# Kernel optimization log

Measured on AMD Instinct MI355X. Metric: run time of the kernel, lower is better.

The kernel has to match this reference:

```python
import jax, jax.numpy as jnp
import numpy as np
import math

THETA = 10000.0
NUM_HEADS = 16


def apply_rope(x, pos, theta):
    # x: [B, H, S, Dh], pos: [S]
    d_k = x.shape[-1]
    inv_freq = theta ** (-jnp.arange(0, d_k, 2, dtype=x.dtype) / d_k)  # [Dh/2]
    angles = pos.astype(x.dtype)[:, None] * inv_freq  # [S, Dh/2]
    cos = jnp.cos(angles)
    sin = jnp.sin(angles)
    x_even = x[..., ::2]
    x_odd = x[..., 1::2]
    out_even = x_even * cos - x_odd * sin
    out_odd = x_even * sin + x_odd * cos
    # interleave back: stack on trailing axis then flatten
    return jnp.stack((out_even, out_odd), axis=-1).reshape(x.shape)


def setup_inputs() -> dict:
    key = jax.random.key(0)
    ks = jax.random.split(key, 5)
    B, S, D = 2, 2048, 1024
    scale = 1.0 / math.sqrt(D)
    return {
        "in_features": jax.random.normal(ks[0], (B, S, D), dtype=jnp.float32),
        "token_positions": jnp.arange(S, dtype=jnp.int64 if jax.config.jax_enable_x64 else jnp.int32),
        "Wq": jax.random.normal(ks[1], (D, D), dtype=jnp.float32) * scale,
        "Wk": jax.random.normal(ks[2], (D, D), dtype=jnp.float32) * scale,
        "Wv": jax.random.normal(ks[3], (D, D), dtype=jnp.float32) * scale,
        "Wo": jax.random.normal(ks[4], (D, D), dtype=jnp.float32) * scale,
    }


def reference(in_features, token_positions, Wq, Wk, Wv, Wo):
    B, S, D = in_features.shape
    H = NUM_HEADS
    Dh = D // H

    def split_heads(x):  # [B,S,D] -> [B,H,S,Dh]
        return x.reshape(B, S, H, Dh).transpose(0, 2, 1, 3)

    # nn.Linear convention: y = x @ W.T
    q = split_heads(in_features @ Wq.T)
    k = split_heads(in_features @ Wk.T)
    v = split_heads(in_features @ Wv.T)

    q = apply_rope(q, token_positions, THETA)
    k = apply_rope(k, token_positions, THETA)

    scores = jnp.einsum('bhqd,bhkd->bhqk', q, k) / jnp.sqrt(jnp.asarray(Dh, q.dtype))
    causal = jnp.tril(jnp.ones((S, S), dtype=bool))
    scores = jnp.where(causal, scores, jnp.asarray(-jnp.inf, scores.dtype))
    weights = jax.nn.softmax(scores, axis=-1)
    out = jnp.einsum('bhqk,bhkd->bhqd', weights, v)  # [B,H,S,Dh]
    out = out.transpose(0, 2, 1, 3).reshape(B, S, D)
    return out @ Wo.T
```

## Files before the change

### kernel.cpp

```cpp
#include <hip/hip_runtime.h>
#include <hip/hip_bf16.h>


typedef __bf16 bf16x8 __attribute__((ext_vector_type(8)));
typedef float floatx4 __attribute__((ext_vector_type(4)));
typedef float floatx16 __attribute__((ext_vector_type(16)));
typedef int intx2 __attribute__((ext_vector_type(2)));

#define MFMA16(A, B, C) __builtin_amdgcn_mfma_f32_16x16x32_bf16((A), (B), (C), 0, 0, 0)
#define MFMA32(A, B, C) __builtin_amdgcn_mfma_f32_32x32x16_bf16((A), (B), (C), 0, 0, 0)

#define S_LEN 2048
#define D_MODEL 1024
#define NHEAD 16
#define DHEAD 64
#define NTOK 4096
#define NEG_SENTINEL (-1.0e30f)
#define QSCALE_LOG2E 0.18033688011112042f

__device__ __forceinline__ short b16(float f) {
  __bf16 h = (__bf16)f;
  union { __bf16 b; short s; } u; u.b = h;
  return u.s;
}
__device__ __forceinline__ unsigned pk2(float x, float y) {
  union { __bf16 b[2]; unsigned u; } t;
  t.b[0] = (__bf16)x; t.b[1] = (__bf16)y;
  return t.u;
}
__device__ __forceinline__ bf16x8 ld_frag(const short* p) {
  return *(const bf16x8*)p;
}
__device__ __forceinline__ void gl2lds16(const short* g, short* l) {
  __builtin_amdgcn_global_load_lds(
      (const __attribute__((address_space(1))) unsigned int*)g,
      (__attribute__((address_space(3))) unsigned int*)l, 16, 0, 0);
}
__device__ __forceinline__ float max3f(float a, float b, float c) {
  return fmaxf(fmaxf(a, b), c);
}

__global__ __launch_bounds__(256) void prep_kernel(
    const float* __restrict__ x, const float* __restrict__ wq,
    const float* __restrict__ wk, const float* __restrict__ wv,
    short* __restrict__ xb, short* __restrict__ wqb,
    short* __restrict__ wkb, short* __restrict__ wvb,
    float2* __restrict__ tab) {
  const int y = blockIdx.y;
  if (y == 4) {
    int i = blockIdx.x * 256 + threadIdx.x;
    int s = i >> 5, p = i & 31;
    float inv_freq = __expf(-0.28782313662425575f * (float)p);
    float ang = (float)s * inv_freq;
    float sn, c;
    sincosf(ang, &sn, &c);
    tab[i] = make_float2(c, sn);
    return;
  }
  const float* src = (y == 0) ? x : (y == 1) ? wq : (y == 2) ? wk : wv;
  short* dst = (y == 0) ? xb : (y == 1) ? wqb : (y == 2) ? wkb : wvb;
  const int n4 = ((y == 0) ? NTOK * D_MODEL : D_MODEL * D_MODEL) >> 2;
  for (int i = blockIdx.x * 256 + threadIdx.x; i < n4; i += gridDim.x * 256) {
    float4 v = ((const float4*)src)[i];
    short4 o;
    o.x = b16(v.x); o.y = b16(v.y); o.z = b16(v.z); o.w = b16(v.w);
    ((short4*)dst)[i] = o;
  }
}

__global__ __launch_bounds__(256) void qkv_rope_kernel(
    const short* __restrict__ xb,
    const short* __restrict__ Wqb, const short* __restrict__ Wkb,
    const short* __restrict__ Wvb,
    const float2* __restrict__ ropetab,
    short* __restrict__ qws, short* __restrict__ kws, short* __restrict__ vtws) {
  __shared__ __align__(16) short SM[4 * 64 * 72];
  short* As = SM;
  short* Bs = SM + 128 * 64;

  const int tid = threadIdx.x;
  const int lane = tid & 63;
  const int wv = tid >> 6;
  const int col = lane & 15, quad = lane >> 4;
  const int half = lane >> 5, l31 = lane & 31;
  const int wr = wv >> 1, wc = wv & 1;
  const int gemm = blockIdx.y;
  const int bm = blockIdx.x >> 3;
  const int bn = blockIdx.x & 7;
  const short* W = (gemm == 0) ? Wqb : (gemm == 1) ? Wkb : Wvb;

  const int srow8 = lane >> 3;
  const int scolsw = ((lane & 7) ^ srow8) * 8;
  const short* gAa[4]; short* lAa[4];
  const short* gBa[4]; short* lBa[4];
#pragma unroll
  for (int g = 0; g < 2; ++g)
#pragma unroll
    for (int j = 0; j < 2; ++j) {
      const int idx = g * 2 + j;
      const int r0 = g * 64 + wv * 16 + j * 8;
      gAa[idx] = xb + (size_t)(bm * 128 + r0 + srow8) * D_MODEL + scolsw;
      lAa[idx] = As + r0 * 64;
      gBa[idx] = W + (size_t)(bn * 128 + r0 + srow8) * D_MODEL + scolsw;
      lBa[idx] = Bs + r0 * 64;
    }

  floatx4 acc[4][4];
#pragma unroll
  for (int i = 0; i < 4; ++i)
#pragma unroll
    for (int j = 0; j < 4; ++j) acc[i][j] = (floatx4){0.f, 0.f, 0.f, 0.f};

  const int arow = wr * 64;
  const int brow = wc * 64;

  for (int k0 = 0; k0 < D_MODEL; k0 += 64) {
    __syncthreads();
#pragma unroll
    for (int i = 0; i < 4; ++i) gl2lds16(gAa[i] + k0, lAa[i]);
#pragma unroll
    for (int i = 0; i < 4; ++i) gl2lds16(gBa[i] + k0, lBa[i]);
    __syncthreads();
#pragma unroll
    for (int kk = 0; kk < 2; ++kk) {
      bf16x8 a[4], b[4];
      const int usel = (kk * 4 + quad) ^ (col & 7);
#pragma unroll
      for (int mt = 0; mt < 4; ++mt)
        a[mt] = ld_frag(&As[(arow + mt * 16 + col) * 64 + usel * 8]);
#pragma unroll
      for (int nt = 0; nt < 4; ++nt)
        b[nt] = ld_frag(&Bs[(brow + nt * 16 + col) * 64 + usel * 8]);
#pragma unroll
      for (int mt = 0; mt < 4; ++mt)
#pragma unroll
        for (int nt = 0; nt < 4; ++nt)
          acc[mt][nt] = MFMA16(a[mt], b[nt], acc[mt][nt]);
    }
  }
  __syncthreads();

  const int tm = bm * 2 + wr;
  const int tn = bn * 2 + wc;
  short* Ep = &SM[wv * 64 * 72];
  const int mbase = tm * 64;
  const int bb = mbase >> 11;
  const int s0 = mbase & (S_LEN - 1);

  if (gemm == 2) {
#pragma unroll
    for (int mt = 0; mt < 4; ++mt)
#pragma unroll
      for (int nt = 0; nt < 4; ++nt) {
        int nl = nt * 16 + col;
#pragma unroll
        for (int r = 0; r < 4; ++r)
          Ep[nl * 72 + mt * 16 + quad * 4 + r] = b16(acc[mt][nt][r]);
      }
    short* vb2 = vtws + (size_t)(bb * NHEAD + tn) * S_LEN * DHEAD;
    const int vtile = s0 >> 6;
#pragma unroll
    for (int dt = 0; dt < 2; ++dt) {
      const int4* src = (const int4*)&Ep[(dt * 32 + l31) * 72];
      int4* dst = (int4*)(vb2 + (size_t)(vtile * 8 + dt) * 512);
#pragma unroll
      for (int kc = 0; kc < 4; ++kc)
        dst[kc * 2 * 64 + lane] = src[kc * 2 + half];
    }
  } else {
    short* outp = (gemm == 0) ? qws : kws;
    const float qscale = (gemm == 0) ? QSCALE_LOG2E : 1.0f;
#pragma unroll
    for (int nt = 0; nt < 4; ++nt) {
      int nl = nt * 16 + col;
      const float2* tp = ropetab + (nl >> 1);
#pragma unroll
      for (int mt = 0; mt < 4; ++mt)
#pragma unroll
        for (int r = 0; r < 4; ++r) {
          int ml = mt * 16 + quad * 4 + r;
          float2 cs = tp[(size_t)(s0 + ml) * 32];
          float val = acc[mt][nt][r];
          float partner = __shfl_xor(val, 1);
          float o = ((nl & 1) == 0) ? (val * cs.x - partner * cs.y)
                                    : (partner * cs.y + val * cs.x);
          Ep[ml * 72 + nl] = b16(o * qscale);
        }
    }
    short* ob2 = outp + (size_t)(bb * NHEAD + tn) * S_LEN * DHEAD;
    const int kgrp0 = s0 >> 5;
#pragma unroll
    for (int g2 = 0; g2 < 2; ++g2) {
      const int4* src = (const int4*)&Ep[(g2 * 32 + l31) * 72];
      int4* dst = (int4*)(ob2 + (size_t)((kgrp0 + g2) * 4) * 512);
#pragma unroll
      for (int kc = 0; kc < 4; ++kc)
        dst[kc * 64 + lane] = src[kc * 2 + half];
    }
  }
}

__global__ __launch_bounds__(256) void attn_kernel(
    const short* __restrict__ qws, const short* __restrict__ kws,
    const short* __restrict__ vtws, short* __restrict__ att) {
  const int tid = threadIdx.x;
  const int wv = tid >> 6;
  const int lane = tid & 63;
  const int half = lane >> 5, l31 = lane & 31;
  const int bh = blockIdx.x & 31;
  const int b = bh >> 4, h = bh & 15;
  const int qt = 63 - (blockIdx.x >> 5);
  const int q0 = qt * 32;

  __shared__ float ml[2][4][32];
  __shared__ float Obuf[4][64][33];

  const short* qbase = qws + (size_t)(b * NHEAD + h) * S_LEN * DHEAD;
  const short* kbase = kws + (size_t)(b * NHEAD + h) * S_LEN * DHEAD;
  const short* vbase = vtws + (size_t)(b * NHEAD + h) * S_LEN * DHEAD;

  bf16x8 qf[4];
#pragma unroll
  for (int kc = 0; kc < 4; ++kc)
    qf[kc] = ld_frag(qbase + (size_t)(qt * 4 + kc) * 512 + lane * 8);

  float m_i = NEG_SENTINEL, l_i = 0.f;
  floatx16 ot[2] = {};

  const int nit = (q0 + 32 + 63) >> 6;

  bf16x8 kfA[2][4];
  auto loadK = [&](int tkt) {
#pragma unroll
    for (int s = 0; s < 2; ++s) {
      if (tkt + s * 32 <= q0 + 31) {
        const short* kr = kbase + (size_t)(((tkt >> 5) + s) * 4) * 512 + lane * 8;
#pragma unroll
        for (int kc = 0; kc < 4; ++kc) kfA[s][kc] = ld_frag(kr + kc * 512);
      }
    }
  };

  int it = wv;
  if (it < nit) loadK(it * 64);

  for (; it < nit; it += 4) {
    const int kt = it * 64;
    bf16x8 vf[4][2];
    {
      const short* vr = vbase + (size_t)(kt >> 6) * 8 * 512 + lane * 8;
#pragma unroll
      for (int kc = 0; kc < 4; ++kc)
#pragma unroll
        for (int dt = 0; dt < 2; ++dt)
          vf[kc][dt] = ld_frag(vr + (size_t)(kc * 2 + dt) * 512);
    }
    floatx16 sc[2];
#pragma unroll
    for (int s = 0; s < 2; ++s) {
      if (kt + s * 32 <= q0 + 31) {
        floatx16 a = {};
#pragma unroll
        for (int kc = 0; kc < 4; ++kc) a = MFMA32(kfA[s][kc], qf[kc], a);
        sc[s] = a;
      } else {
#pragma unroll
        for (int rg = 0; rg < 16; ++rg) sc[s][rg] = NEG_SENTINEL;
      }
    }
    if (it + 4 < nit) loadK((it + 4) * 64);

    if (kt + 63 > q0) {
      const int lim = q0 + l31 - kt;
#pragma unroll
      for (int s = 0; s < 2; ++s)
#pragma unroll
        for (int rg = 0; rg < 16; ++rg) {
          int rel = s * 32 + (rg & 3) + 8 * (rg >> 2) + 4 * half;
          if (rel > lim) sc[s][rg] = NEG_SENTINEL;
        }
    }
    float u[11];
#pragma unroll
    for (int j = 0; j < 10; ++j)
      u[j] = max3f(((const float*)&sc[0])[3 * j],
                   ((const float*)&sc[0])[3 * j + 1],
                   ((const float*)&sc[0])[3 * j + 2]);
    u[10] = fmaxf(((const float*)&sc[0])[30], ((const float*)&sc[0])[31]);
    float w0 = max3f(u[0], u[1], u[2]);
    float w1 = max3f(u[3], u[4], u[5]);
    float w2 = max3f(u[6], u[7], u[8]);
    float w3 = fmaxf(u[9], u[10]);
    float rm = fmaxf(fmaxf(w0, w1), fmaxf(w2, w3));

    if (!__all(rm <= m_i + 8.0f)) {
      float rmf = fmaxf(rm, __shfl_xor(rm, 32));
      float mnew = fmaxf(m_i, rmf);
      float alpha = exp2f(m_i - mnew);
      m_i = mnew;
      l_i *= alpha;
#pragma unroll
      for (int dt = 0; dt < 2; ++dt)
#pragma unroll
        for (int rg = 0; rg < 16; ++rg) ot[dt][rg] *= alpha;
    }

    unsigned pw[8][2];
    float rsp[8];
#pragma unroll
    for (int s = 0; s < 2; ++s)
#pragma unroll
      for (int g = 0; g < 4; ++g) {
        float p0 = exp2f(sc[s][4 * g + 0] - m_i);
        float p1 = exp2f(sc[s][4 * g + 1] - m_i);
        float p2 = exp2f(sc[s][4 * g + 2] - m_i);
        float p3 = exp2f(sc[s][4 * g + 3] - m_i);
        rsp[s * 4 + g] = (p0 + p1) + (p2 + p3);
        pw[s * 4 + g][0] = pk2(p0, p1);
        pw[s * 4 + g][1] = pk2(p2, p3);
      }
    float rs = ((rsp[0] + rsp[1]) + (rsp[2] + rsp[3])) +
               ((rsp[4] + rsp[5]) + (rsp[6] + rsp[7]));
    rs += __shfl_xor(rs, 32);
    l_i += rs;

#pragma unroll
    for (int kc = 0; kc < 4; ++kc) {
      intx2 s01 = __builtin_amdgcn_permlane32_swap(
          (int)pw[2 * kc][0], (int)pw[2 * kc + 1][0], false, false);
      intx2 s23 = __builtin_amdgcn_permlane32_swap(
          (int)pw[2 * kc][1], (int)pw[2 * kc + 1][1], false, false);
      union { unsigned u[4]; bf16x8 f; } fr;
      fr.u[0] = (unsigned)s01[0]; fr.u[1] = (unsigned)s23[0];
      fr.u[2] = (unsigned)s01[1]; fr.u[3] = (unsigned)s23[1];
#pragma unroll
      for (int dt = 0; dt < 2; ++dt)
        ot[dt] = MFMA32(vf[kc][dt], fr.f, ot[dt]);
    }
  }

  ml[0][wv][l31] = m_i;
  ml[1][wv][l31] = l_i;
  __syncthreads();
  float m0 = ml[0][0][l31], m1 = ml[0][1][l31];
  float m2 = ml[0][2][l31], m3 = ml[0][3][l31];
  float mtot = fmaxf(fmaxf(m0, m1), fmaxf(m2, m3));
  float sw = exp2f(m_i - mtot);

#pragma unroll
  for (int dt = 0; dt < 2; ++dt)
#pragma unroll
    for (int rg = 0; rg < 16; ++rg) {
      int d = dt * 32 + (rg & 3) + 8 * (rg >> 2) + 4 * half;
      Obuf[wv][d][l31] = ot[dt][rg] * sw;
    }
  __syncthreads();

  const int q = tid >> 3;
  const int d0 = (tid & 7) * 8;
  float mm0 = ml[0][0][q], mm1 = ml[0][1][q], mm2 = ml[0][2][q], mm3 = ml[0][3][q];
  float mt2 = fmaxf(fmaxf(mm0, mm1), fmaxf(mm2, mm3));
  float lt = ml[1][0][q] * exp2f(mm0 - mt2) + ml[1][1][q] * exp2f(mm1 - mt2) +
             ml[1][2][q] * exp2f(mm2 - mt2) + ml[1][3][q] * exp2f(mm3 - mt2);
  float inv = 1.0f / lt;
  union { bf16x8 hh; int4 i4; } cv;
#pragma unroll
  for (int i = 0; i < 8; ++i) {
    float v = ((Obuf[0][d0 + i][q] + Obuf[1][d0 + i][q]) +
               (Obuf[2][d0 + i][q] + Obuf[3][d0 + i][q]));
    cv.hh[i] = (__bf16)(v * inv);
  }
  int4* dst = (int4*)(att + (size_t)(b * S_LEN + q0 + q) * D_MODEL + h * DHEAD + d0);
  *dst = cv.i4;
}

__global__ __launch_bounds__(256) void out_gemm_kernel(
    const short* __restrict__ att, const float* __restrict__ Wo,
    float* __restrict__ out) {
  __shared__ __align__(16) short As[128 * 64];
  __shared__ __align__(16) short Bs[64 * 64];

  const int tid = threadIdx.x;
  const int lane = tid & 63;
  const int wv = tid >> 6;
  const int col = lane & 15, quad = lane >> 4;
  const int wr = wv >> 1, wc = wv & 1;
  const int bm = blockIdx.x >> 4;
  const int bn = blockIdx.x & 15;

  const int srow8 = lane >> 3;
  const int scolsw = ((lane & 7) ^ srow8) * 8;
  const short* gAa[4]; short* lAa[4];
#pragma unroll
  for (int g = 0; g < 2; ++g)
#pragma unroll
    for (int j = 0; j < 2; ++j) {
      const int idx = g * 2 + j;
      const int r0 = g * 64 + wv * 16 + j * 8;
      gAa[idx] = att + (size_t)(bm * 128 + r0 + srow8) * D_MODEL + scolsw;
      lAa[idx] = As + r0 * 64;
    }

  const int browB = tid >> 2;
  const int bc0 = (tid & 3) * 16;
  const float* gBf = Wo + (size_t)(bn * 64 + browB) * D_MODEL + bc0;
  short* lBw0 = Bs + browB * 64 + (((tid & 3) * 2) ^ (browB & 7)) * 8;
  short* lBw1 = Bs + browB * 64 + (((tid & 3) * 2 + 1) ^ (browB & 7)) * 8;

  floatx4 acc[4][2];
#pragma unroll
  for (int i = 0; i < 4; ++i)
#pragma unroll
    for (int j = 0; j < 2; ++j) acc[i][j] = (floatx4){0.f, 0.f, 0.f, 0.f};

  const int arow = wr * 64;
  const int brow = wc * 32;

  for (int k0 = 0; k0 < D_MODEL; k0 += 64) {
    float4 w0 = *(const float4*)(gBf + k0);
    float4 w1 = *(const float4*)(gBf + k0 + 4);
    float4 w2 = *(const float4*)(gBf + k0 + 8);
    float4 w3 = *(const float4*)(gBf + k0 + 12);
    __syncthreads();
#pragma unroll
    for (int i = 0; i < 4; ++i) gl2lds16(gAa[i] + k0, lAa[i]);
    union { unsigned u[4]; int4 i4; } b0, b1;
    b0.u[0] = pk2(w0.x, w0.y); b0.u[1] = pk2(w0.z, w0.w);
    b0.u[2] = pk2(w1.x, w1.y); b0.u[3] = pk2(w1.z, w1.w);
    b1.u[0] = pk2(w2.x, w2.y); b1.u[1] = pk2(w2.z, w2.w);
    b1.u[2] = pk2(w3.x, w3.y); b1.u[3] = pk2(w3.z, w3.w);
    *(int4*)lBw0 = b0.i4;
    *(int4*)lBw1 = b1.i4;
    __syncthreads();
#pragma unroll
    for (int kk = 0; kk < 2; ++kk) {
      bf16x8 a[4], b[2];
      const int usel = (kk * 4 + quad) ^ (col & 7);
#pragma unroll
      for (int mt = 0; mt < 4; ++mt)
        a[mt] = ld_frag(&As[(arow + mt * 16 + col) * 64 + usel * 8]);
#pragma unroll
      for (int nt = 0; nt < 2; ++nt)
        b[nt] = ld_frag(&Bs[(brow + nt * 16 + col) * 64 + usel * 8]);
#pragma unroll
      for (int mt = 0; mt < 4; ++mt)
#pragma unroll
        for (int nt = 0; nt < 2; ++nt)
          acc[mt][nt] = MFMA16(a[mt], b[nt], acc[mt][nt]);
    }
  }

#pragma unroll
  for (int mt = 0; mt < 4; ++mt)
#pragma unroll
    for (int nt = 0; nt < 2; ++nt) {
      int n = bn * 64 + wc * 32 + nt * 16 + col;
#pragma unroll
      for (int r = 0; r < 4; ++r) {
        int m = bm * 128 + wr * 64 + mt * 16 + quad * 4 + r;
        out[(size_t)m * D_MODEL + n] = acc[mt][nt][r];
      }
    }
}

extern "C" void kernel_launch(void* const* d_in, const int* in_sizes, int n_in,
                              void* d_out, int out_size, void* d_ws, size_t ws_size,
                              hipStream_t stream) {
  const float* x  = (const float*)d_in[0];
  const float* Wq = (const float*)d_in[2];
  const float* Wk = (const float*)d_in[3];
  const float* Wv = (const float*)d_in[4];
  const float* Wo = (const float*)d_in[5];
  float* out = (float*)d_out;

  const size_t TENS = (size_t)NTOK * D_MODEL;
  const size_t WELEM = (size_t)D_MODEL * D_MODEL;

  short* qws  = (short*)d_out;
  short* xb   = (short*)d_out + TENS;
  short* kws  = (short*)d_ws;
  short* vtws = kws + TENS;
  short* attws = vtws + TENS;
  short* wqb = attws;
  short* wkb = wqb + WELEM;
  short* wvb = wkb + WELEM;
  float2* ropetab = (float2*)(wvb + WELEM);

  prep_kernel<<<dim3(256, 5), 256, 0, stream>>>(x, Wq, Wk, Wv, xb, wqb, wkb, wvb, ropetab);
  qkv_rope_kernel<<<dim3(256, 3), 256, 0, stream>>>(xb, wqb, wkb, wvb, ropetab, qws, kws, vtws);
  attn_kernel<<<dim3(2048), 256, 0, stream>>>(qws, kws, vtws, attws);
  out_gemm_kernel<<<dim3(512), 256, 0, stream>>>(attws, Wo, out);
}
```

Baseline: 191.3 us.

## Split attention inner loop into two 32-key phases and halve LDS output buffer

The 64-key iteration of the attention kernel is restructured into two 32-key sub-phases, each computing scores, online softmax and PV MFMAs separately. V fragments are loaded per phase, which lowers live register pressure and interleaves the next K prefetch with each half. The cross-wave output reduction now uses a two-slot LDS buffer with an extra barrier and accumulate step, halving shared memory. The cost is more softmax rescale checks, extra shuffles per tile and one more synchronisation.

```diff
diff --git a/kernel.cpp b/kernel.cpp
--- a/kernel.cpp
+++ b/kernel.cpp
@@ -213,7 +213,7 @@
   const int q0 = qt * 32;
 
   __shared__ float ml[2][4][32];
-  __shared__ float Obuf[4][64][33];
+  __shared__ float Obuf[2][64][33];
 
   const short* qbase = qws + (size_t)(b * NHEAD + h) * S_LEN * DHEAD;
   const short* kbase = kws + (size_t)(b * NHEAD + h) * S_LEN * DHEAD;
@@ -230,69 +230,28 @@
   const int nit = (q0 + 32 + 63) >> 6;
 
   bf16x8 kfA[2][4];
-  auto loadK = [&](int tkt) {
-#pragma unroll
-    for (int s = 0; s < 2; ++s) {
-      if (tkt + s * 32 <= q0 + 31) {
-        const short* kr = kbase + (size_t)(((tkt >> 5) + s) * 4) * 512 + lane * 8;
-#pragma unroll
-        for (int kc = 0; kc < 4; ++kc) kfA[s][kc] = ld_frag(kr + kc * 512);
-      }
+  auto loadKs = [&](int s, int tkt) {
+    if (tkt + s * 32 <= q0 + 31) {
+      const short* kr = kbase + (size_t)(((tkt >> 5) + s) * 4) * 512 + lane * 8;
+#pragma unroll
+      for (int kc = 0; kc < 4; ++kc) kfA[s][kc] = ld_frag(kr + kc * 512);
     }
   };
 
-  int it = wv;
-  if (it < nit) loadK(it * 64);
-
-  for (; it < nit; it += 4) {
-    const int kt = it * 64;
-    bf16x8 vf[4][2];
-    {
-      const short* vr = vbase + (size_t)(kt >> 6) * 8 * 512 + lane * 8;
-#pragma unroll
-      for (int kc = 0; kc < 4; ++kc)
-#pragma unroll
-        for (int dt = 0; dt < 2; ++dt)
-          vf[kc][dt] = ld_frag(vr + (size_t)(kc * 2 + dt) * 512);
-    }
-    floatx16 sc[2];
-#pragma unroll
-    for (int s = 0; s < 2; ++s) {
-      if (kt + s * 32 <= q0 + 31) {
-        floatx16 a = {};
-#pragma unroll
-        for (int kc = 0; kc < 4; ++kc) a = MFMA32(kfA[s][kc], qf[kc], a);
-        sc[s] = a;
-      } else {
-#pragma unroll
-        for (int rg = 0; rg < 16; ++rg) sc[s][rg] = NEG_SENTINEL;
-      }
-    }
-    if (it + 4 < nit) loadK((it + 4) * 64);
-
-    if (kt + 63 > q0) {
-      const int lim = q0 + l31 - kt;
-#pragma unroll
-      for (int s = 0; s < 2; ++s)
-#pragma unroll
-        for (int rg = 0; rg < 16; ++rg) {
-          int rel = s * 32 + (rg & 3) + 8 * (rg >> 2) + 4 * half;
-          if (rel > lim) sc[s][rg] = NEG_SENTINEL;
-        }
-    }
-    float u[11];
-#pragma unroll
-    for (int j = 0; j < 10; ++j)
-      u[j] = max3f(((const float*)&sc[0])[3 * j],
-                   ((const float*)&sc[0])[3 * j + 1],
-                   ((const float*)&sc[0])[3 * j + 2]);
-    u[10] = fmaxf(((const float*)&sc[0])[30], ((const float*)&sc[0])[31]);
-    float w0 = max3f(u[0], u[1], u[2]);
-    float w1 = max3f(u[3], u[4], u[5]);
-    float w2 = max3f(u[6], u[7], u[8]);
-    float w3 = fmaxf(u[9], u[10]);
-    float rm = fmaxf(fmaxf(w0, w1), fmaxf(w2, w3));
-
+  auto phase = [&](floatx16 sc, int kbase_rel, const short* vr) {
+    bf16x8 vfp[2][2];
+#pragma unroll
+    for (int kcg = 0; kcg < 2; ++kcg)
+#pragma unroll
+      for (int dt = 0; dt < 2; ++dt)
+        vfp[kcg][dt] = ld_frag(vr + (size_t)(kcg * 2 + dt) * 512);
+    const float* sf = (const float*)&sc;
+    float u0 = max3f(sf[0], sf[1], sf[2]);
+    float u1 = max3f(sf[3], sf[4], sf[5]);
+    float u2 = max3f(sf[6], sf[7], sf[8]);
+    float u3 = max3f(sf[9], sf[10], sf[11]);
+    float u4 = max3f(sf[12], sf[13], sf[14]);
+    float rm = fmaxf(max3f(u0, u1, u2), max3f(u3, u4, sf[15]));
     if (!__all(rm <= m_i + 8.0f)) {
       float rmf = fmaxf(rm, __shfl_xor(rm, 32));
       float mnew = fmaxf(m_i, rmf);
@@ -304,38 +263,75 @@
 #pragma unroll
         for (int rg = 0; rg < 16; ++rg) ot[dt][rg] *= alpha;
     }
-
-    unsigned pw[8][2];
-    float rsp[8];
-#pragma unroll
-    for (int s = 0; s < 2; ++s)
-#pragma unroll
-      for (int g = 0; g < 4; ++g) {
-        float p0 = exp2f(sc[s][4 * g + 0] - m_i);
-        float p1 = exp2f(sc[s][4 * g + 1] - m_i);
-        float p2 = exp2f(sc[s][4 * g + 2] - m_i);
-        float p3 = exp2f(sc[s][4 * g + 3] - m_i);
-        rsp[s * 4 + g] = (p0 + p1) + (p2 + p3);
-        pw[s * 4 + g][0] = pk2(p0, p1);
-        pw[s * 4 + g][1] = pk2(p2, p3);
-      }
-    float rs = ((rsp[0] + rsp[1]) + (rsp[2] + rsp[3])) +
-               ((rsp[4] + rsp[5]) + (rsp[6] + rsp[7]));
+    unsigned pw[4][2];
+    float rsp[4];
+#pragma unroll
+    for (int g = 0; g < 4; ++g) {
+      float p0 = exp2f(sc[4 * g + 0] - m_i);
+      float p1 = exp2f(sc[4 * g + 1] - m_i);
+      float p2 = exp2f(sc[4 * g + 2] - m_i);
+      float p3 = exp2f(sc[4 * g + 3] - m_i);
+      rsp[g] = (p0 + p1) + (p2 + p3);
+      pw[g][0] = pk2(p0, p1);
+      pw[g][1] = pk2(p2, p3);
+    }
+    float rs = (rsp[0] + rsp[1]) + (rsp[2] + rsp[3]);
     rs += __shfl_xor(rs, 32);
     l_i += rs;
-
-#pragma unroll
-    for (int kc = 0; kc < 4; ++kc) {
+#pragma unroll
+    for (int kcg = 0; kcg < 2; ++kcg) {
       intx2 s01 = __builtin_amdgcn_permlane32_swap(
-          (int)pw[2 * kc][0], (int)pw[2 * kc + 1][0], false, false);
+          (int)pw[2 * kcg][0], (int)pw[2 * kcg + 1][0], false, false);
       intx2 s23 = __builtin_amdgcn_permlane32_swap(
-          (int)pw[2 * kc][1], (int)pw[2 * kc + 1][1], false, false);
+          (int)pw[2 * kcg][1], (int)pw[2 * kcg + 1][1], false, false);
       union { unsigned u[4]; bf16x8 f; } fr;
       fr.u[0] = (unsigned)s01[0]; fr.u[1] = (unsigned)s23[0];
       fr.u[2] = (unsigned)s01[1]; fr.u[3] = (unsigned)s23[1];
 #pragma unroll
       for (int dt = 0; dt < 2; ++dt)
-        ot[dt] = MFMA32(vf[kc][dt], fr.f, ot[dt]);
+        ot[dt] = MFMA32(vfp[kcg][dt], fr.f, ot[dt]);
+    }
+    (void)kbase_rel;
+  };
+
+  int it = wv;
+  if (it < nit) { loadKs(0, it * 64); loadKs(1, it * 64); }
+
+  for (; it < nit; it += 4) {
+    const int kt = it * 64;
+    const bool havenext = (it + 4 < nit);
+    const short* vr0 = vbase + (size_t)(kt >> 6) * 8 * 512 + lane * 8;
+
+    {
+      floatx16 a = {};
+#pragma unroll
+      for (int kc = 0; kc < 4; ++kc) a = MFMA32(kfA[0][kc], qf[kc], a);
+      if (havenext) loadKs(0, (it + 4) * 64);
+      if (kt + 31 > q0) {
+        const int lim = q0 + l31 - kt;
+#pragma unroll
+        for (int rg = 0; rg < 16; ++rg) {
+          int rel = (rg & 3) + 8 * (rg >> 2) + 4 * half;
+          if (rel > lim) a[rg] = NEG_SENTINEL;
+        }
+      }
+      phase(a, kt, vr0);
+    }
+
+    if (kt + 32 <= q0 + 31) {
+      floatx16 a = {};
+#pragma unroll
+      for (int kc = 0; kc < 4; ++kc) a = MFMA32(kfA[1][kc], qf[kc], a);
+      if (havenext) loadKs(1, (it + 4) * 64);
+      if (kt + 63 > q0) {
+        const int lim = q0 + l31 - kt;
+#pragma unroll
+        for (int rg = 0; rg < 16; ++rg) {
+          int rel = 32 + (rg & 3) + 8 * (rg >> 2) + 4 * half;
+          if (rel > lim) a[rg] = NEG_SENTINEL;
+        }
+      }
+      phase(a, kt + 32, vr0 + (size_t)4 * 512);
     }
   }
 
@@ -347,13 +343,25 @@
   float mtot = fmaxf(fmaxf(m0, m1), fmaxf(m2, m3));
   float sw = exp2f(m_i - mtot);
 
-#pragma unroll
-  for (int dt = 0; dt < 2; ++dt)
-#pragma unroll
-    for (int rg = 0; rg < 16; ++rg) {
-      int d = dt * 32 + (rg & 3) + 8 * (rg >> 2) + 4 * half;
-      Obuf[wv][d][l31] = ot[dt][rg] * sw;
-    }
+  if (wv < 2) {
+#pragma unroll
+    for (int dt = 0; dt < 2; ++dt)
+#pragma unroll
+      for (int rg = 0; rg < 16; ++rg) {
+        int d = dt * 32 + (rg & 3) + 8 * (rg >> 2) + 4 * half;
+        Obuf[wv][d][l31] = ot[dt][rg] * sw;
+      }
+  }
+  __syncthreads();
+  if (wv >= 2) {
+#pragma unroll
+    for (int dt = 0; dt < 2; ++dt)
+#pragma unroll
+      for (int rg = 0; rg < 16; ++rg) {
+        int d = dt * 32 + (rg & 3) + 8 * (rg >> 2) + 4 * half;
+        Obuf[wv - 2][d][l31] += ot[dt][rg] * sw;
+      }
+  }
   __syncthreads();
 
   const int q = tid >> 3;
@@ -366,8 +374,7 @@
   union { bf16x8 hh; int4 i4; } cv;
 #pragma unroll
   for (int i = 0; i < 8; ++i) {
-    float v = ((Obuf[0][d0 + i][q] + Obuf[1][d0 + i][q]) +
-               (Obuf[2][d0 + i][q] + Obuf[3][d0 + i][q]));
+    float v = Obuf[0][d0 + i][q] + Obuf[1][d0 + i][q];
     cv.hh[i] = (__bf16)(v * inv);
   }
   int4* dst = (int4*)(att + (size_t)(b * S_LEN + q0 + q) * D_MODEL + h * DHEAD + d0);
```

Result: slower. 198.4 us (+3.7%).
